# Kernel optimization log

Measured on AMD Instinct MI355X. Metric: run time of the kernel, lower is better.

## Reference

```python
import jax, jax.numpy as jnp
import numpy as np

D_MODEL = 1024
N_HEADS = 16
D_HEAD = D_MODEL // N_HEADS
EPS = 1e-5
NEG = -1.0e9


def layer_norm(x, w, b=None):
    mu = jnp.mean(x, axis=-1, keepdims=True)
    var = jnp.mean((x - mu) ** 2, axis=-1, keepdims=True)
    y = (x - mu) * jax.lax.rsqrt(var + EPS) * w
    return y + b if b is not None else y


def rope_cos_sin(L, dh, dtype):
    inv_freq = 1.0 / (10000.0 ** (jnp.arange(0, dh, 2, dtype=jnp.float32) / dh))
    freqs = jnp.arange(L, dtype=jnp.float32)[:, None] * inv_freq[None, :]  # [L, dh/2]
    emb = jnp.concatenate([freqs, freqs], axis=-1)  # [L, dh]
    return jnp.cos(emb).astype(dtype)[None, :, None, :], jnp.sin(emb).astype(dtype)[None, :, None, :]


def apply_rope(x, cos, sin):
    # x: [B, L, H, dh]; rotate_half = cat(-x2, x1)
    d = x.shape[-1] // 2
    x1, x2 = x[..., :d], x[..., d:]
    rot = jnp.concatenate([-x2, x1], axis=-1)
    return x * cos + rot * sin


def setup_inputs() -> dict:
    key = jax.random.key(0)
    ks = jax.random.split(key, 8)
    B, L, D = 2, 2048, D_MODEL
    x = jax.random.normal(ks[0], (B, L, D), dtype=jnp.float32)
    attention_mask = jnp.ones((B, L), dtype=bool)
    chain_id = jnp.sort(jax.random.randint(ks[1], (B, L), 0, 4), axis=-1).astype(jnp.int32)
    attn_bias = jax.random.normal(ks[2], (B, 1, L, L), dtype=jnp.float32) * 0.05
    s = 0.02
    return {
        "x": x,
        "attention_mask": attention_mask,
        "chain_id": chain_id,
        "attn_bias": attn_bias,
        "ln1_w": jnp.ones((D,), jnp.float32),
        "ln1_b": jnp.zeros((D,), jnp.float32),
        "Wqkv": jax.random.normal(ks[3], (D, 3 * D), jnp.float32) * s,
        "q_ln_w": jnp.ones((D,), jnp.float32),
        "k_ln_w": jnp.ones((D,), jnp.float32),
        "Wout": jax.random.normal(ks[4], (D, D), jnp.float32) * s,
    }


def reference(x, attention_mask, chain_id, attn_bias, ln1_w, ln1_b, Wqkv, q_ln_w, k_ln_w, Wout):
    B, L, D = x.shape
    H, dh = N_HEADS, D_HEAD
    # fused LN + QKV projection (Linear has no bias)
    qkv = layer_norm(x, ln1_w, ln1_b) @ Wqkv  # [B, L, 3D]
    q, k, v = jnp.split(qkv, 3, axis=-1)
    # qk layernorm (bias=False -> scale only)
    q = layer_norm(q, q_ln_w)
    k = layer_norm(k, k_ln_w)
    # rotary on [B, L, H, dh]
    q = q.reshape(B, L, H, dh)
    k = k.reshape(B, L, H, dh)
    cos, sin = rope_cos_sin(L, dh, q.dtype)
    q = apply_rope(q, cos, sin)
    k = apply_rope(k, cos, sin)
    v = v.reshape(B, L, H, dh)
    # chain mask & padding mask -> additive bias [B,1,L,L]
    mask = (chain_id[:, :, None] == chain_id[:, None, :]) \
        & attention_mask[:, :, None] & attention_mask[:, None, :]
    mask_bias = jnp.where(mask[:, None, :, :], 0.0, NEG).astype(q.dtype)
    scale = 1.0 / np.sqrt(dh)
    scores = jnp.einsum("blhd,bshd->bhls", q, k) * scale + mask_bias + attn_bias
    attn_weight = jax.nn.softmax(scores, axis=-1)  # [B,H,L,L]
    ctx = jnp.einsum("bhls,bshd->blhd", attn_weight, v).reshape(B, L, D)
    out = ctx @ Wout
    return attn_weight, out
```

## Files before the change

### kernel.cpp

```cpp
#include <hip/hip_runtime.h>


#define DEVI __device__ __forceinline__

typedef _Float16 f16;
typedef f16 f16x4 __attribute__((ext_vector_type(4)));
typedef f16 f16x8 __attribute__((ext_vector_type(8)));
typedef float f32x4 __attribute__((ext_vector_type(4)));

constexpr int Bsz = 2, Lq = 2048, Dm = 1024, Hh = 16;
constexpr int BHn = Bsz * Hh;
constexpr int ROWS = Bsz * Lq;
constexpr long long ATTN_N = (long long)BHn * Lq * Lq;

constexpr size_t OFF_XN  = 0;
constexpr size_t OFF_WQT = OFF_XN  + (size_t)4096*1024*2;
constexpr size_t OFF_WOT = OFF_WQT + (size_t)3072*1024*2;
constexpr size_t OFF_QKV = OFF_WOT + (size_t)1024*1024*2;
constexpr size_t OFF_Q   = OFF_QKV + (size_t)4096*3072*4;
constexpr size_t OFF_K   = OFF_Q   + (size_t)32*2048*64*2;
constexpr size_t OFF_VT  = OFF_K   + (size_t)32*2048*64*2;
constexpr size_t OFF_CTX = OFF_VT  + (size_t)32*64*2048*2;
constexpr size_t OFF_COS = OFF_CTX + (size_t)4096*1024*2;
constexpr size_t OFF_SIN = OFF_COS + (size_t)2048*32*4;
constexpr size_t WS_NEED = OFF_SIN + (size_t)2048*32*4;

DEVI float wsum(float v) {
#pragma unroll
  for (int o = 32; o; o >>= 1) v += __shfl_xor(v, o);
  return v;
}
DEVI float wmaxr(float v) {
#pragma unroll
  for (int o = 32; o; o >>= 1) v = fmaxf(v, __shfl_xor(v, o));
  return v;
}
DEVI f32x4 zero4() { f32x4 z; z[0]=0.f; z[1]=0.f; z[2]=0.f; z[3]=0.f; return z; }

__global__ __launch_bounds__(256) void k_ln1(const float* __restrict__ x,
    const float* __restrict__ w, const float* __restrict__ bb,
    f16* __restrict__ xn) {
  const int row = blockIdx.x, t = threadIdx.x;
  const float4 v = ((const float4*)(x + (size_t)row * Dm))[t];
  float s  = v.x + v.y + v.z + v.w;
  float s2 = v.x*v.x + v.y*v.y + v.z*v.z + v.w*v.w;
  s = wsum(s); s2 = wsum(s2);
  __shared__ float red[8];
  const int lane = t & 63, wid = t >> 6;
  if (!lane) { red[wid] = s; red[4 + wid] = s2; }
  __syncthreads();
  s  = red[0] + red[1] + red[2] + red[3];
  s2 = red[4] + red[5] + red[6] + red[7];
  const float mu = s * (1.f / Dm);
  const float rs = rsqrtf(s2 * (1.f / Dm) - mu * mu + 1e-5f);
  const float4 wv = ((const float4*)w)[t];
  const float4 bv = ((const float4*)bb)[t];
  f16x4 o;
  o[0] = (f16)((v.x - mu) * rs * wv.x + bv.x);
  o[1] = (f16)((v.y - mu) * rs * wv.y + bv.y);
  o[2] = (f16)((v.z - mu) * rs * wv.z + bv.z);
  o[3] = (f16)((v.w - mu) * rs * wv.w + bv.w);
  ((f16x4*)(xn + (size_t)row * Dm))[t] = o;
}

__global__ __launch_bounds__(256) void k_rope_tab(float* __restrict__ ct,
                                                  float* __restrict__ st) {
  const int idx = blockIdx.x * 256 + threadIdx.x;
  const int l = idx >> 5, i = idx & 31;
  const float inv = (float)(1.0 / pow(10000.0, (double)(2 * i) / 64.0));
  const float ph = (float)l * inv;
  ct[idx] = cosf(ph);
  st[idx] = sinf(ph);
}

__global__ __launch_bounds__(256) void k_transpose(const float* __restrict__ src,
    f16* __restrict__ dst, int sstride, int dstride,
    long long sbstride, long long dbstride) {
  __shared__ float tile[64][65];
  const int c0 = blockIdx.x * 64, r0 = blockIdx.y * 64;
  const float* s = src + (long long)blockIdx.z * sbstride;
  f16* d = dst + (long long)blockIdx.z * dbstride;
  const int t = threadIdx.x;
#pragma unroll
  for (int i = 0; i < 16; i++) {
    const int idx = t + i * 256, r = idx >> 6, c = idx & 63;
    tile[r][c] = s[(size_t)(r0 + r) * sstride + c0 + c];
  }
  __syncthreads();
#pragma unroll
  for (int i = 0; i < 16; i++) {
    const int idx = t + i * 256, r = idx >> 6, c = idx & 63;
    d[(size_t)(c0 + r) * dstride + r0 + c] = (f16)tile[c][r];
  }
}

template <int BM, int BN, int WR, int WC, bool AF32>
DEVI void gemm_acc(const void* __restrict__ Ag_, int lda,
                   const f16* __restrict__ Bg, int ldb, int nk,
                   char* ldsA, char* ldsB,
                   f32x4 acc[BM / WR / 16][BN / WC / 16]) {
  constexpr int MR = BM / WR / 16, NR = BN / WC / 16;
  const int t = threadIdx.x, lane = t & 63, wid = t >> 6;
  const int wr = wid / WC, wc = wid % WC;
  const int r16 = lane & 15, q = lane >> 4;
  for (int k0 = 0; k0 < nk; ++k0) {
#pragma unroll
    for (int s = 0; s < BM * 8 / 256; ++s) {
      const int sl = t + s * 256;
      const int row = sl >> 3, c16 = sl & 7;
      const int phys = (sl * 16) ^ ((row & 7) << 4);
      if constexpr (AF32) {
        const float* g = (const float*)Ag_ + (size_t)row * lda + k0 * 64 + c16 * 8;
        const float4 lo = *(const float4*)g;
        const float4 hi = *(const float4*)(g + 4);
        f16x8 h;
        h[0]=(f16)lo.x; h[1]=(f16)lo.y; h[2]=(f16)lo.z; h[3]=(f16)lo.w;
        h[4]=(f16)hi.x; h[5]=(f16)hi.y; h[6]=(f16)hi.z; h[7]=(f16)hi.w;
        *(f16x8*)(ldsA + phys) = h;
      } else {
        const f16* g = (const f16*)Ag_ + (size_t)row * lda + k0 * 64 + c16 * 8;
        *(int4*)(ldsA + phys) = *(const int4*)g;
      }
    }
#pragma unroll
    for (int s = 0; s < BN * 8 / 256; ++s) {
      const int sl = t + s * 256;
      const int row = sl >> 3, c16 = sl & 7;
      const int phys = (sl * 16) ^ ((row & 7) << 4);
      const f16* g = Bg + (size_t)row * ldb + k0 * 64 + c16 * 8;
      *(int4*)(ldsB + phys) = *(const int4*)g;
    }
    __syncthreads();
    f16x8 af[MR][2], bf[NR][2];
#pragma unroll
    for (int ks = 0; ks < 2; ++ks) {
#pragma unroll
      for (int m = 0; m < MR; m++) {
        const int row = wr * (BM / WR) + m * 16 + r16;
        const int lg = row * 128 + ks * 64 + q * 16;
        af[m][ks] = *(const f16x8*)(ldsA + (lg ^ ((row & 7) << 4)));
      }
#pragma unroll
      for (int n = 0; n < NR; n++) {
        const int row = wc * (BN / WC) + n * 16 + r16;
        const int lg = row * 128 + ks * 64 + q * 16;
        bf[n][ks] = *(const f16x8*)(ldsB + (lg ^ ((row & 7) << 4)));
      }
    }
#pragma unroll
    for (int ks = 0; ks < 2; ++ks)
#pragma unroll
      for (int m = 0; m < MR; m++)
#pragma unroll
        for (int n = 0; n < NR; n++)
          acc[m][n] = __builtin_amdgcn_mfma_f32_16x16x32_f16(af[m][ks], bf[n][ks],
                                                             acc[m][n], 0, 0, 0);
    __syncthreads();
  }
}

__global__ __launch_bounds__(256) void k_gemm_qkv(const f16* __restrict__ xn,
    const f16* __restrict__ wT, float* __restrict__ qkv) {
  __shared__ alignas(16) char lds[2 * 128 * 64 * 2];
  f32x4 acc[4][4];
#pragma unroll
  for (int m = 0; m < 4; m++)
#pragma unroll
    for (int n = 0; n < 4; n++) acc[m][n] = zero4();
  const int bm = blockIdx.x, bn = blockIdx.y;
  gemm_acc<128, 128, 2, 2, false>(xn + (size_t)bm * 128 * 1024, 1024,
                                  wT + (size_t)bn * 128 * 1024, 1024, 16,
                                  lds, lds + 128 * 64 * 2, acc);
  const int lane = threadIdx.x & 63, wid = threadIdx.x >> 6;
  const int wr = wid >> 1, wc = wid & 1;
#pragma unroll
  for (int m = 0; m < 4; m++)
#pragma unroll
    for (int n = 0; n < 4; n++) {
      const int grow = bm * 128 + wr * 64 + m * 16 + (lane >> 4) * 4;
      const int gcol = bn * 128 + wc * 64 + n * 16 + (lane & 15);
#pragma unroll
      for (int r = 0; r < 4; r++)
        qkv[(size_t)(grow + r) * 3072 + gcol] = acc[m][n][r];
    }
}

__global__ __launch_bounds__(256) void k_qkln_rope(const float* __restrict__ qkv,
    const float* __restrict__ qw, const float* __restrict__ kw,
    const float* __restrict__ ct, const float* __restrict__ st,
    f16* __restrict__ Q, f16* __restrict__ Kk) {
  const int row = blockIdx.x, t = threadIdx.x;
  const int b = row >> 11, l = row & 2047;
  const float4 qv = ((const float4*)(qkv + (size_t)row * 3072))[t];
  const float4 kv = ((const float4*)(qkv + (size_t)row * 3072 + 1024))[t];
  float qs = qv.x + qv.y + qv.z + qv.w;
  float qs2 = qv.x*qv.x + qv.y*qv.y + qv.z*qv.z + qv.w*qv.w;
  float ks_ = kv.x + kv.y + kv.z + kv.w;
  float ks2 = kv.x*kv.x + kv.y*kv.y + kv.z*kv.z + kv.w*kv.w;
  qs = wsum(qs); qs2 = wsum(qs2); ks_ = wsum(ks_); ks2 = wsum(ks2);
  __shared__ float red[16];
  const int lane = t & 63, wid = t >> 6;
  if (!lane) { red[wid] = qs; red[4+wid] = qs2; red[8+wid] = ks_; red[12+wid] = ks2; }
  __syncthreads();
  qs  = red[0]+red[1]+red[2]+red[3];   qs2 = red[4]+red[5]+red[6]+red[7];
  ks_ = red[8]+red[9]+red[10]+red[11]; ks2 = red[12]+red[13]+red[14]+red[15];
  const float qmu = qs * (1.f/1024), qrs = rsqrtf(qs2*(1.f/1024) - qmu*qmu + 1e-5f);
  const float kmu = ks_ * (1.f/1024), krs = rsqrtf(ks2*(1.f/1024) - kmu*kmu + 1e-5f);
  __shared__ float qn[1024], kn[1024];
  const float4 qwv = ((const float4*)qw)[t], kwv = ((const float4*)kw)[t];
  float4 qnn, knn;
  qnn.x = (qv.x-qmu)*qrs*qwv.x; qnn.y = (qv.y-qmu)*qrs*qwv.y;
  qnn.z = (qv.z-qmu)*qrs*qwv.z; qnn.w = (qv.w-qmu)*qrs*qwv.w;
  knn.x = (kv.x-kmu)*krs*kwv.x; knn.y = (kv.y-kmu)*krs*kwv.y;
  knn.z = (kv.z-kmu)*krs*kwv.z; knn.w = (kv.w-kmu)*krs*kwv.w;
  ((float4*)qn)[t] = qnn;
  ((float4*)kn)[t] = knn;
  __syncthreads();
  const int d0 = 4 * t, h = d0 >> 6, dd0 = d0 & 63;
  f16x4 qo, ko;
#pragma unroll
  for (int j = 0; j < 4; j++) {
    const int d = d0 + j, dd = d & 63, p = dd & 31;
    const float c = ct[l * 32 + p], s = st[l * 32 + p];
    const float q1 = qn[d], k1 = kn[d];
    const float qr = (dd < 32) ? -qn[d + 32] : qn[d - 32];
    const float kr = (dd < 32) ? -kn[d + 32] : kn[d - 32];
    qo[j] = (f16)(q1 * c + qr * s);
    ko[j] = (f16)(k1 * c + kr * s);
  }
  const size_t base = (((size_t)(b * 16 + h) * 2048) + l) * 64 + dd0;
  *(f16x4*)(Q + base) = qo;
  *(f16x4*)(Kk + base) = ko;
}

__global__ __launch_bounds__(256) void k_gemm_scores(const f16* __restrict__ Q,
    const f16* __restrict__ Kk, const int* __restrict__ chain,
    const float* __restrict__ bias, float* __restrict__ attn) {
  __shared__ alignas(16) char lds[2 * 128 * 64 * 2];
  __shared__ int cidr[128], cidc[128];
  f32x4 acc[4][4];
#pragma unroll
  for (int m = 0; m < 4; m++)
#pragma unroll
    for (int n = 0; n < 4; n++) acc[m][n] = zero4();
  const int bm = blockIdx.x, bn = blockIdx.y, bh = blockIdx.z;
  const int b = bh >> 4;
  gemm_acc<128, 128, 2, 2, false>(Q + ((size_t)bh * 2048 + bm * 128) * 64, 64,
                                  Kk + ((size_t)bh * 2048 + bn * 128) * 64, 64, 1,
                                  lds, lds + 128 * 64 * 2, acc);
  const int t = threadIdx.x;
  if (t < 128) cidr[t] = chain[b * 2048 + bm * 128 + t];
  else cidc[t - 128] = chain[b * 2048 + bn * 128 + (t - 128)];
  __syncthreads();
  const int lane = t & 63, wid = t >> 6, wr = wid >> 1, wc = wid & 1;
#pragma unroll
  for (int m = 0; m < 4; m++)
#pragma unroll
    for (int n = 0; n < 4; n++) {
      const int lr0 = wr * 64 + m * 16 + (lane >> 4) * 4;
      const int lc = wc * 64 + n * 16 + (lane & 15);
      const int s = bn * 128 + lc;
      const int cs = cidc[lc];
#pragma unroll
      for (int r = 0; r < 4; r++) {
        const int l = bm * 128 + lr0 + r;
        float v = acc[m][n][r] * 0.125f + bias[((size_t)b * 2048 + l) * 2048 + s];
        if (cidr[lr0 + r] != cs) v -= 1e9f;
        attn[((size_t)bh * 2048 + l) * 2048 + s] = v;
      }
    }
}

__global__ __launch_bounds__(256) void k_softmax(float* __restrict__ attn) {
  float* p = attn + (size_t)blockIdx.x * 2048;
  const int t = threadIdx.x;
  float4 a0 = ((const float4*)p)[t];
  float4 a1 = ((const float4*)p)[t + 256];
  float m = fmaxf(fmaxf(fmaxf(a0.x, a0.y), fmaxf(a0.z, a0.w)),
                  fmaxf(fmaxf(a1.x, a1.y), fmaxf(a1.z, a1.w)));
  m = wmaxr(m);
  __shared__ float red[4];
  const int lane = t & 63, wid = t >> 6;
  if (!lane) red[wid] = m;
  __syncthreads();
  m = fmaxf(fmaxf(red[0], red[1]), fmaxf(red[2], red[3]));
  float4 e0, e1;
  e0.x = __expf(a0.x - m); e0.y = __expf(a0.y - m);
  e0.z = __expf(a0.z - m); e0.w = __expf(a0.w - m);
  e1.x = __expf(a1.x - m); e1.y = __expf(a1.y - m);
  e1.z = __expf(a1.z - m); e1.w = __expf(a1.w - m);
  float s = e0.x+e0.y+e0.z+e0.w + e1.x+e1.y+e1.z+e1.w;
  s = wsum(s);
  __syncthreads();
  if (!lane) red[wid] = s;
  __syncthreads();
  s = red[0] + red[1] + red[2] + red[3];
  const float inv = 1.f / s;
  e0.x *= inv; e0.y *= inv; e0.z *= inv; e0.w *= inv;
  e1.x *= inv; e1.y *= inv; e1.z *= inv; e1.w *= inv;
  ((float4*)p)[t] = e0;
  ((float4*)p)[t + 256] = e1;
}

__global__ __launch_bounds__(256) void k_gemm_pv(const float* __restrict__ attn,
    const f16* __restrict__ Vt, f16* __restrict__ ctx) {
  __shared__ alignas(16) char lds[128 * 64 * 2 + 64 * 64 * 2];
  f32x4 acc[2][4];
#pragma unroll
  for (int m = 0; m < 2; m++)
#pragma unroll
    for (int n = 0; n < 4; n++) acc[m][n] = zero4();
  const int bm = blockIdx.x, bh = blockIdx.z;
  gemm_acc<128, 64, 4, 1, true>(attn + ((size_t)bh * 2048 + bm * 128) * 2048, 2048,
                                Vt + (size_t)bh * 64 * 2048, 2048, 32,
                                lds, lds + 128 * 64 * 2, acc);
  const int lane = threadIdx.x & 63, wid = threadIdx.x >> 6;
  const int b = bh >> 4, h = bh & 15;
#pragma unroll
  for (int m = 0; m < 2; m++)
#pragma unroll
    for (int n = 0; n < 4; n++) {
      const int l0 = bm * 128 + wid * 32 + m * 16 + (lane >> 4) * 4;
      const int dd = n * 16 + (lane & 15);
#pragma unroll
      for (int r = 0; r < 4; r++)
        ctx[(((size_t)b * 2048 + (l0 + r)) * 16 + h) * 64 + dd] = (f16)acc[m][n][r];
    }
}

__global__ __launch_bounds__(256) void k_gemm_proj(const f16* __restrict__ ctx,
    const f16* __restrict__ wT, float* __restrict__ out) {
  __shared__ alignas(16) char lds[2 * 128 * 64 * 2];
  f32x4 acc[4][4];
#pragma unroll
  for (int m = 0; m < 4; m++)
#pragma unroll
    for (int n = 0; n < 4; n++) acc[m][n] = zero4();
  const int bm = blockIdx.x, bn = blockIdx.y;
  gemm_acc<128, 128, 2, 2, false>(ctx + (size_t)bm * 128 * 1024, 1024,
                                  wT + (size_t)bn * 128 * 1024, 1024, 16,
                                  lds, lds + 128 * 64 * 2, acc);
  const int lane = threadIdx.x & 63, wid = threadIdx.x >> 6;
  const int wr = wid >> 1, wc = wid & 1;
#pragma unroll
  for (int m = 0; m < 4; m++)
#pragma unroll
    for (int n = 0; n < 4; n++) {
      const int grow = bm * 128 + wr * 64 + m * 16 + (lane >> 4) * 4;
      const int gcol = bn * 128 + wc * 64 + n * 16 + (lane & 15);
#pragma unroll
      for (int r = 0; r < 4; r++)
        out[(size_t)(grow + r) * 1024 + gcol] = acc[m][n][r];
    }
}

extern "C" void kernel_launch(void* const* d_in, const int* in_sizes, int n_in,
                              void* d_out, int out_size, void* d_ws, size_t ws_size,
                              hipStream_t stream) {
  const float* x    = (const float*)d_in[0];
  const int*   chain = (const int*)d_in[2];
  const float* bias = (const float*)d_in[3];
  const float* ln1w = (const float*)d_in[4];
  const float* ln1b = (const float*)d_in[5];
  const float* wqkv = (const float*)d_in[6];
  const float* qlnw = (const float*)d_in[7];
  const float* klnw = (const float*)d_in[8];
  const float* wout = (const float*)d_in[9];

  float* attn = (float*)d_out;
  float* outp = attn + ATTN_N;

  char* ws = (char*)d_ws;
  f16*   xn    = (f16*)(ws + OFF_XN);
  f16*   wqkvT = (f16*)(ws + OFF_WQT);
  f16*   woutT = (f16*)(ws + OFF_WOT);
  float* qkv   = (float*)(ws + OFF_QKV);
  f16*   Qh    = (f16*)(ws + OFF_Q);
  f16*   Kh    = (f16*)(ws + OFF_K);
  f16*   Vt    = (f16*)(ws + OFF_VT);
  f16*   ctx   = (f16*)(ws + OFF_CTX);
  float* ct    = (float*)(ws + OFF_COS);
  float* st    = (float*)(ws + OFF_SIN);

  k_ln1<<<ROWS, 256, 0, stream>>>(x, ln1w, ln1b, xn);
  k_rope_tab<<<(2048 * 32) / 256, 256, 0, stream>>>(ct, st);
  k_transpose<<<dim3(3072 / 64, 1024 / 64, 1), 256, 0, stream>>>(
      wqkv, wqkvT, 3072, 1024, 0, 0);
  k_transpose<<<dim3(1024 / 64, 1024 / 64, 1), 256, 0, stream>>>(
      wout, woutT, 1024, 1024, 0, 0);
  k_gemm_qkv<<<dim3(4096 / 128, 3072 / 128), 256, 0, stream>>>(xn, wqkvT, qkv);
  k_qkln_rope<<<ROWS, 256, 0, stream>>>(qkv, qlnw, klnw, ct, st, Qh, Kh);
  k_transpose<<<dim3(1024 / 64, 2048 / 64, 2), 256, 0, stream>>>(
      qkv + 2048, Vt, 3072, 2048, (long long)2048 * 3072, (long long)1024 * 2048);
  k_gemm_scores<<<dim3(16, 16, 32), 256, 0, stream>>>(Qh, Kh, chain, bias, attn);
  k_softmax<<<BHn * Lq, 256, 0, stream>>>(attn);
  k_gemm_pv<<<dim3(16, 1, 32), 256, 0, stream>>>(attn, Vt, ctx);
  k_gemm_proj<<<dim3(4096 / 128, 1024 / 128), 256, 0, stream>>>(ctx, woutT, outp);
}
```

Measured before the change: 1.111 ms.

## Fuse score computation and softmax into two-pass online max/sum attention kernels

Replaces the scores GEMM plus separate softmax kernel with two kernels. The first streams K tiles to compute the per-row running max and sum online. The second recomputes QK, applies bias and mask, and writes normalized probabilities directly. This removes the write-then-read-then-write round trip of the full fp32 score matrix, in exchange for computing QK and reading bias twice. It also uses a much smaller grid with a serial loop over key tiles.

```diff
diff --git a/kernel.cpp b/kernel.cpp
--- a/kernel.cpp
+++ b/kernel.cpp
@@ -23,16 +23,12 @@
 constexpr size_t OFF_CTX = OFF_VT  + (size_t)32*64*2048*2;
 constexpr size_t OFF_COS = OFF_CTX + (size_t)4096*1024*2;
 constexpr size_t OFF_SIN = OFF_COS + (size_t)2048*32*4;
-constexpr size_t WS_NEED = OFF_SIN + (size_t)2048*32*4;
+constexpr size_t OFF_M   = OFF_SIN + (size_t)2048*32*4;
+constexpr size_t OFF_L   = OFF_M   + (size_t)32*2048*4;
 
 DEVI float wsum(float v) {
 #pragma unroll
   for (int o = 32; o; o >>= 1) v += __shfl_xor(v, o);
-  return v;
-}
-DEVI float wmaxr(float v) {
-#pragma unroll
-  for (int o = 32; o; o >>= 1) v = fmaxf(v, __shfl_xor(v, o));
   return v;
 }
 DEVI f32x4 zero4() { f32x4 z; z[0]=0.f; z[1]=0.f; z[2]=0.f; z[3]=0.f; return z; }
@@ -233,73 +229,151 @@
   *(f16x4*)(Kk + base) = ko;
 }
 
-__global__ __launch_bounds__(256) void k_gemm_scores(const f16* __restrict__ Q,
-    const f16* __restrict__ Kk, const int* __restrict__ chain,
-    const float* __restrict__ bias, float* __restrict__ attn) {
-  __shared__ alignas(16) char lds[2 * 128 * 64 * 2];
+DEVI void stage_tile64(const f16* __restrict__ g, char* lds) {
+  const int t = threadIdx.x;
+#pragma unroll
+  for (int s = 0; s < 4; ++s) {
+    const int sl = t + s * 256;
+    const int row = sl >> 3, c16 = sl & 7;
+    const int phys = (sl * 16) ^ ((row & 7) << 4);
+    *(int4*)(lds + phys) = *(const int4*)(g + (size_t)row * 64 + c16 * 8);
+  }
+}
+DEVI f16x8 ldsfrag(const char* lds, int row, int ks, int q) {
+  const int lg = row * 128 + ks * 64 + q * 16;
+  return *(const f16x8*)(lds + (lg ^ ((row & 7) << 4)));
+}
+DEVI void attn_qk_tile(const char* ldsQ, const char* ldsK, int wid, int lo, int q,
+                       f32x4 acc[2][8]) {
+#pragma unroll
+  for (int m = 0; m < 2; m++)
+#pragma unroll
+    for (int n = 0; n < 8; n++) acc[m][n] = zero4();
+#pragma unroll
+  for (int ks = 0; ks < 2; ++ks) {
+    const f16x8 a0 = ldsfrag(ldsQ, wid * 32 + lo, ks, q);
+    const f16x8 a1 = ldsfrag(ldsQ, wid * 32 + 16 + lo, ks, q);
+#pragma unroll
+    for (int n = 0; n < 8; ++n) {
+      const f16x8 bf = ldsfrag(ldsK, n * 16 + lo, ks, q);
+      acc[0][n] = __builtin_amdgcn_mfma_f32_16x16x32_f16(a0, bf, acc[0][n], 0, 0, 0);
+      acc[1][n] = __builtin_amdgcn_mfma_f32_16x16x32_f16(a1, bf, acc[1][n], 0, 0, 0);
+    }
+  }
+}
+
+__global__ __launch_bounds__(256) void k_attn_ml(const f16* __restrict__ Qh,
+    const f16* __restrict__ Kh, const int* __restrict__ chain,
+    const float* __restrict__ bias, float* __restrict__ marr,
+    float* __restrict__ larr) {
+  __shared__ alignas(16) char ldsQ[128 * 64 * 2];
+  __shared__ alignas(16) char ldsK[128 * 64 * 2];
   __shared__ int cidr[128], cidc[128];
-  f32x4 acc[4][4];
-#pragma unroll
-  for (int m = 0; m < 4; m++)
-#pragma unroll
-    for (int n = 0; n < 4; n++) acc[m][n] = zero4();
-  const int bm = blockIdx.x, bn = blockIdx.y, bh = blockIdx.z;
-  const int b = bh >> 4;
-  gemm_acc<128, 128, 2, 2, false>(Q + ((size_t)bh * 2048 + bm * 128) * 64, 64,
-                                  Kk + ((size_t)bh * 2048 + bn * 128) * 64, 64, 1,
-                                  lds, lds + 128 * 64 * 2, acc);
-  const int t = threadIdx.x;
+  const int bm = blockIdx.x, bh = blockIdx.y, b = bh >> 4;
+  const int t = threadIdx.x, lane = t & 63, wid = t >> 6;
+  const int lo = lane & 15, q = lane >> 4;
+  stage_tile64(Qh + ((size_t)bh * 2048 + bm * 128) * 64, ldsQ);
   if (t < 128) cidr[t] = chain[b * 2048 + bm * 128 + t];
-  else cidc[t - 128] = chain[b * 2048 + bn * 128 + (t - 128)];
-  __syncthreads();
-  const int lane = t & 63, wid = t >> 6, wr = wid >> 1, wc = wid & 1;
-#pragma unroll
-  for (int m = 0; m < 4; m++)
-#pragma unroll
-    for (int n = 0; n < 4; n++) {
-      const int lr0 = wr * 64 + m * 16 + (lane >> 4) * 4;
-      const int lc = wc * 64 + n * 16 + (lane & 15);
-      const int s = bn * 128 + lc;
-      const int cs = cidc[lc];
+  float mr[2][4], lr[2][4];
+#pragma unroll
+  for (int m = 0; m < 2; m++)
+#pragma unroll
+    for (int r = 0; r < 4; r++) { mr[m][r] = -__builtin_inff(); lr[m][r] = 0.f; }
+  for (int bn = 0; bn < 16; ++bn) {
+    __syncthreads();
+    stage_tile64(Kh + ((size_t)bh * 2048 + bn * 128) * 64, ldsK);
+    if (t < 128) cidc[t] = chain[b * 2048 + bn * 128 + t];
+    __syncthreads();
+    f32x4 acc[2][8];
+    attn_qk_tile(ldsQ, ldsK, wid, lo, q, acc);
+    const int s0 = bn * 128;
+#pragma unroll
+    for (int m = 0; m < 2; m++)
 #pragma unroll
       for (int r = 0; r < 4; r++) {
-        const int l = bm * 128 + lr0 + r;
-        float v = acc[m][n][r] * 0.125f + bias[((size_t)b * 2048 + l) * 2048 + s];
-        if (cidr[lr0 + r] != cs) v -= 1e9f;
-        attn[((size_t)bh * 2048 + l) * 2048 + s] = v;
-      }
-    }
-}
-
-__global__ __launch_bounds__(256) void k_softmax(float* __restrict__ attn) {
-  float* p = attn + (size_t)blockIdx.x * 2048;
-  const int t = threadIdx.x;
-  float4 a0 = ((const float4*)p)[t];
-  float4 a1 = ((const float4*)p)[t + 256];
-  float m = fmaxf(fmaxf(fmaxf(a0.x, a0.y), fmaxf(a0.z, a0.w)),
-                  fmaxf(fmaxf(a1.x, a1.y), fmaxf(a1.z, a1.w)));
-  m = wmaxr(m);
-  __shared__ float red[4];
-  const int lane = t & 63, wid = t >> 6;
-  if (!lane) red[wid] = m;
-  __syncthreads();
-  m = fmaxf(fmaxf(red[0], red[1]), fmaxf(red[2], red[3]));
-  float4 e0, e1;
-  e0.x = __expf(a0.x - m); e0.y = __expf(a0.y - m);
-  e0.z = __expf(a0.z - m); e0.w = __expf(a0.w - m);
-  e1.x = __expf(a1.x - m); e1.y = __expf(a1.y - m);
-  e1.z = __expf(a1.z - m); e1.w = __expf(a1.w - m);
-  float s = e0.x+e0.y+e0.z+e0.w + e1.x+e1.y+e1.z+e1.w;
-  s = wsum(s);
-  __syncthreads();
-  if (!lane) red[wid] = s;
-  __syncthreads();
-  s = red[0] + red[1] + red[2] + red[3];
-  const float inv = 1.f / s;
-  e0.x *= inv; e0.y *= inv; e0.z *= inv; e0.w *= inv;
-  e1.x *= inv; e1.y *= inv; e1.z *= inv; e1.w *= inv;
-  ((float4*)p)[t] = e0;
-  ((float4*)p)[t + 256] = e1;
+        const int lloc = wid * 32 + m * 16 + q * 4 + r;
+        const int l = bm * 128 + lloc;
+        const int cr = cidr[lloc];
+        const float* bp = bias + ((size_t)b * 2048 + l) * 2048 + s0 + lo;
+        float lg[8];
+        float tmax = -__builtin_inff();
+#pragma unroll
+        for (int n = 0; n < 8; ++n) {
+          float v = acc[m][n][r] * 0.125f + bp[n * 16];
+          if (cr != cidc[n * 16 + lo]) v -= 1e9f;
+          lg[n] = v;
+          tmax = fmaxf(tmax, v);
+        }
+#pragma unroll
+        for (int o = 1; o < 16; o <<= 1) tmax = fmaxf(tmax, __shfl_xor(tmax, o));
+        const float nm = fmaxf(mr[m][r], tmax);
+        float ss = 0.f;
+#pragma unroll
+        for (int n = 0; n < 8; ++n) ss += __expf(lg[n] - nm);
+#pragma unroll
+        for (int o = 1; o < 16; o <<= 1) ss += __shfl_xor(ss, o);
+        lr[m][r] = lr[m][r] * __expf(mr[m][r] - nm) + ss;
+        mr[m][r] = nm;
+      }
+  }
+  if (lo == 0) {
+#pragma unroll
+    for (int m = 0; m < 2; m++)
+#pragma unroll
+      for (int r = 0; r < 4; r++) {
+        const int l = bm * 128 + wid * 32 + m * 16 + q * 4 + r;
+        marr[(size_t)bh * 2048 + l] = mr[m][r];
+        larr[(size_t)bh * 2048 + l] = lr[m][r];
+      }
+  }
+}
+
+__global__ __launch_bounds__(256) void k_attn_pw(const f16* __restrict__ Qh,
+    const f16* __restrict__ Kh, const int* __restrict__ chain,
+    const float* __restrict__ bias, const float* __restrict__ marr,
+    const float* __restrict__ larr, float* __restrict__ attn) {
+  __shared__ alignas(16) char ldsQ[128 * 64 * 2];
+  __shared__ alignas(16) char ldsK[128 * 64 * 2];
+  __shared__ int cidr[128], cidc[128];
+  const int bm = blockIdx.x, bh = blockIdx.y, b = bh >> 4;
+  const int t = threadIdx.x, lane = t & 63, wid = t >> 6;
+  const int lo = lane & 15, q = lane >> 4;
+  stage_tile64(Qh + ((size_t)bh * 2048 + bm * 128) * 64, ldsQ);
+  if (t < 128) cidr[t] = chain[b * 2048 + bm * 128 + t];
+  float mr[2][4], il[2][4];
+#pragma unroll
+  for (int m = 0; m < 2; m++)
+#pragma unroll
+    for (int r = 0; r < 4; r++) {
+      const int l = bm * 128 + wid * 32 + m * 16 + q * 4 + r;
+      mr[m][r] = marr[(size_t)bh * 2048 + l];
+      il[m][r] = 1.f / larr[(size_t)bh * 2048 + l];
+    }
+  for (int bn = 0; bn < 16; ++bn) {
+    __syncthreads();
+    stage_tile64(Kh + ((size_t)bh * 2048 + bn * 128) * 64, ldsK);
+    if (t < 128) cidc[t] = chain[b * 2048 + bn * 128 + t];
+    __syncthreads();
+    f32x4 acc[2][8];
+    attn_qk_tile(ldsQ, ldsK, wid, lo, q, acc);
+    const int s0 = bn * 128;
+#pragma unroll
+    for (int m = 0; m < 2; m++)
+#pragma unroll
+      for (int r = 0; r < 4; r++) {
+        const int lloc = wid * 32 + m * 16 + q * 4 + r;
+        const int l = bm * 128 + lloc;
+        const int cr = cidr[lloc];
+        const float* bp = bias + ((size_t)b * 2048 + l) * 2048 + s0 + lo;
+        float* op = attn + ((size_t)bh * 2048 + l) * 2048 + s0 + lo;
+#pragma unroll
+        for (int n = 0; n < 8; ++n) {
+          float v = acc[m][n][r] * 0.125f + bp[n * 16];
+          if (cr != cidc[n * 16 + lo]) v -= 1e9f;
+          op[n * 16] = __expf(v - mr[m][r]) * il[m][r];
+        }
+      }
+  }
 }
 
 __global__ __launch_bounds__(256) void k_gemm_pv(const float* __restrict__ attn,
@@ -381,6 +455,8 @@
   f16*   ctx   = (f16*)(ws + OFF_CTX);
   float* ct    = (float*)(ws + OFF_COS);
   float* st    = (float*)(ws + OFF_SIN);
+  float* marr  = (float*)(ws + OFF_M);
+  float* larr  = (float*)(ws + OFF_L);
 
   k_ln1<<<ROWS, 256, 0, stream>>>(x, ln1w, ln1b, xn);
   k_rope_tab<<<(2048 * 32) / 256, 256, 0, stream>>>(ct, st);
@@ -392,8 +468,8 @@
   k_qkln_rope<<<ROWS, 256, 0, stream>>>(qkv, qlnw, klnw, ct, st, Qh, Kh);
   k_transpose<<<dim3(1024 / 64, 2048 / 64, 2), 256, 0, stream>>>(
       qkv + 2048, Vt, 3072, 2048, (long long)2048 * 3072, (long long)1024 * 2048);
-  k_gemm_scores<<<dim3(16, 16, 32), 256, 0, stream>>>(Qh, Kh, chain, bias, attn);
-  k_softmax<<<BHn * Lq, 256, 0, stream>>>(attn);
+  k_attn_ml<<<dim3(16, 32), 256, 0, stream>>>(Qh, Kh, chain, bias, marr, larr);
+  k_attn_pw<<<dim3(16, 32), 256, 0, stream>>>(Qh, Kh, chain, bias, marr, larr, attn);
   k_gemm_pv<<<dim3(16, 1, 32), 256, 0, stream>>>(attn, Vt, ctx);
   k_gemm_proj<<<dim3(4096 / 128, 1024 / 128), 256, 0, stream>>>(ctx, woutT, outp);
 }
```

After: 1.340 ms. 20.6% more time.

## Fuse scores, softmax and PV into two-pass flash-style attention kernels

Applied to the files above, without the earlier changes.

Replaces the separate scores GEMM, softmax and PV GEMM with two kernels. The first computes the per-row running max and sum, and the second recomputes scores, writes the normalized attention weights once, and accumulates P·V in registers. This removes the round trips that write, reread and rewrite the large fp32 attention matrix. The cost is recomputing QK^T, and both new kernels read K, V and the bias straight from global memory without LDS staging, with a grid of only 512 blocks. It also swaps the MFMA operand order so GEMM epilogues can store float4 rows, and routes ctx through fp32 into the projection.

```diff
diff --git a/kernel.cpp b/kernel.cpp
--- a/kernel.cpp
+++ b/kernel.cpp
@@ -17,25 +17,33 @@
 constexpr size_t OFF_WQT = OFF_XN  + (size_t)4096*1024*2;
 constexpr size_t OFF_WOT = OFF_WQT + (size_t)3072*1024*2;
 constexpr size_t OFF_QKV = OFF_WOT + (size_t)1024*1024*2;
+constexpr size_t OFF_CTXF = OFF_QKV;
 constexpr size_t OFF_Q   = OFF_QKV + (size_t)4096*3072*4;
 constexpr size_t OFF_K   = OFF_Q   + (size_t)32*2048*64*2;
 constexpr size_t OFF_VT  = OFF_K   + (size_t)32*2048*64*2;
-constexpr size_t OFF_CTX = OFF_VT  + (size_t)32*64*2048*2;
-constexpr size_t OFF_COS = OFF_CTX + (size_t)4096*1024*2;
+constexpr size_t OFF_COS = OFF_VT  + (size_t)32*64*2048*2;
 constexpr size_t OFF_SIN = OFF_COS + (size_t)2048*32*4;
-constexpr size_t WS_NEED = OFF_SIN + (size_t)2048*32*4;
+constexpr size_t OFF_M   = OFF_SIN + (size_t)2048*32*4;
+constexpr size_t OFF_L   = OFF_M   + (size_t)32*2048*4;
 
 DEVI float wsum(float v) {
 #pragma unroll
   for (int o = 32; o; o >>= 1) v += __shfl_xor(v, o);
   return v;
 }
-DEVI float wmaxr(float v) {
-#pragma unroll
-  for (int o = 32; o; o >>= 1) v = fmaxf(v, __shfl_xor(v, o));
-  return v;
-}
 DEVI f32x4 zero4() { f32x4 z; z[0]=0.f; z[1]=0.f; z[2]=0.f; z[3]=0.f; return z; }
+
+DEVI f32x4 mfma32(f16x8 a, f16x8 b, f32x4 c) {
+  return __builtin_amdgcn_mfma_f32_16x16x32_f16(a, b, c, 0, 0, 0);
+}
+DEVI f32x4 mfma16(f16x4 a, f16x4 b, f32x4 c) {
+#if __has_builtin(__builtin_amdgcn_mfma_f32_16x16x16f16)
+  return __builtin_amdgcn_mfma_f32_16x16x16f16(a, b, c, 0, 0, 0);
+#else
+  asm volatile("v_mfma_f32_16x16x16_f16 %0, %1, %2, %0" : "+v"(c) : "v"(a), "v"(b));
+  return c;
+#endif
+}
 
 __global__ __launch_bounds__(256) void k_ln1(const float* __restrict__ x,
     const float* __restrict__ w, const float* __restrict__ bb,
@@ -153,8 +161,7 @@
       for (int m = 0; m < MR; m++)
 #pragma unroll
         for (int n = 0; n < NR; n++)
-          acc[m][n] = __builtin_amdgcn_mfma_f32_16x16x32_f16(af[m][ks], bf[n][ks],
-                                                             acc[m][n], 0, 0, 0);
+          acc[m][n] = mfma32(bf[n][ks], af[m][ks], acc[m][n]);
     __syncthreads();
   }
 }
@@ -173,15 +180,17 @@
                                   lds, lds + 128 * 64 * 2, acc);
   const int lane = threadIdx.x & 63, wid = threadIdx.x >> 6;
   const int wr = wid >> 1, wc = wid & 1;
+  const int xr = lane & 15, q4 = lane >> 4;
 #pragma unroll
   for (int m = 0; m < 4; m++)
 #pragma unroll
     for (int n = 0; n < 4; n++) {
-      const int grow = bm * 128 + wr * 64 + m * 16 + (lane >> 4) * 4;
-      const int gcol = bn * 128 + wc * 64 + n * 16 + (lane & 15);
-#pragma unroll
-      for (int r = 0; r < 4; r++)
-        qkv[(size_t)(grow + r) * 3072 + gcol] = acc[m][n][r];
+      const int grow = bm * 128 + wr * 64 + m * 16 + xr;
+      const int gcol = bn * 128 + wc * 64 + n * 16 + q4 * 4;
+      float4 st4;
+      st4.x = acc[m][n][0]; st4.y = acc[m][n][1];
+      st4.z = acc[m][n][2]; st4.w = acc[m][n][3];
+      *(float4*)(qkv + (size_t)grow * 3072 + gcol) = st4;
     }
 }
 
@@ -233,102 +242,161 @@
   *(f16x4*)(Kk + base) = ko;
 }
 
-__global__ __launch_bounds__(256) void k_gemm_scores(const f16* __restrict__ Q,
-    const f16* __restrict__ Kk, const int* __restrict__ chain,
-    const float* __restrict__ bias, float* __restrict__ attn) {
-  __shared__ alignas(16) char lds[2 * 128 * 64 * 2];
-  __shared__ int cidr[128], cidc[128];
-  f32x4 acc[4][4];
-#pragma unroll
-  for (int m = 0; m < 4; m++)
-#pragma unroll
-    for (int n = 0; n < 4; n++) acc[m][n] = zero4();
-  const int bm = blockIdx.x, bn = blockIdx.y, bh = blockIdx.z;
-  const int b = bh >> 4;
-  gemm_acc<128, 128, 2, 2, false>(Q + ((size_t)bh * 2048 + bm * 128) * 64, 64,
-                                  Kk + ((size_t)bh * 2048 + bn * 128) * 64, 64, 1,
-                                  lds, lds + 128 * 64 * 2, acc);
-  const int t = threadIdx.x;
-  if (t < 128) cidr[t] = chain[b * 2048 + bm * 128 + t];
-  else cidc[t - 128] = chain[b * 2048 + bn * 128 + (t - 128)];
-  __syncthreads();
-  const int lane = t & 63, wid = t >> 6, wr = wid >> 1, wc = wid & 1;
-#pragma unroll
-  for (int m = 0; m < 4; m++)
-#pragma unroll
-    for (int n = 0; n < 4; n++) {
-      const int lr0 = wr * 64 + m * 16 + (lane >> 4) * 4;
-      const int lc = wc * 64 + n * 16 + (lane & 15);
-      const int s = bn * 128 + lc;
-      const int cs = cidc[lc];
-#pragma unroll
-      for (int r = 0; r < 4; r++) {
-        const int l = bm * 128 + lr0 + r;
-        float v = acc[m][n][r] * 0.125f + bias[((size_t)b * 2048 + l) * 2048 + s];
-        if (cidr[lr0 + r] != cs) v -= 1e9f;
-        attn[((size_t)bh * 2048 + l) * 2048 + s] = v;
-      }
-    }
-}
-
-__global__ __launch_bounds__(256) void k_softmax(float* __restrict__ attn) {
-  float* p = attn + (size_t)blockIdx.x * 2048;
-  const int t = threadIdx.x;
-  float4 a0 = ((const float4*)p)[t];
-  float4 a1 = ((const float4*)p)[t + 256];
-  float m = fmaxf(fmaxf(fmaxf(a0.x, a0.y), fmaxf(a0.z, a0.w)),
-                  fmaxf(fmaxf(a1.x, a1.y), fmaxf(a1.z, a1.w)));
-  m = wmaxr(m);
-  __shared__ float red[4];
-  const int lane = t & 63, wid = t >> 6;
-  if (!lane) red[wid] = m;
-  __syncthreads();
-  m = fmaxf(fmaxf(red[0], red[1]), fmaxf(red[2], red[3]));
-  float4 e0, e1;
-  e0.x = __expf(a0.x - m); e0.y = __expf(a0.y - m);
-  e0.z = __expf(a0.z - m); e0.w = __expf(a0.w - m);
-  e1.x = __expf(a1.x - m); e1.y = __expf(a1.y - m);
-  e1.z = __expf(a1.z - m); e1.w = __expf(a1.w - m);
-  float s = e0.x+e0.y+e0.z+e0.w + e1.x+e1.y+e1.z+e1.w;
-  s = wsum(s);
-  __syncthreads();
-  if (!lane) red[wid] = s;
-  __syncthreads();
-  s = red[0] + red[1] + red[2] + red[3];
-  const float inv = 1.f / s;
-  e0.x *= inv; e0.y *= inv; e0.z *= inv; e0.w *= inv;
-  e1.x *= inv; e1.y *= inv; e1.z *= inv; e1.w *= inv;
-  ((float4*)p)[t] = e0;
-  ((float4*)p)[t + 256] = e1;
-}
-
-__global__ __launch_bounds__(256) void k_gemm_pv(const float* __restrict__ attn,
-    const f16* __restrict__ Vt, f16* __restrict__ ctx) {
-  __shared__ alignas(16) char lds[128 * 64 * 2 + 64 * 64 * 2];
-  f32x4 acc[2][4];
+__global__ __launch_bounds__(256) void k_attn_ml(const f16* __restrict__ Qh,
+    const f16* __restrict__ Kh, const int* __restrict__ chain,
+    const float* __restrict__ bias, float* __restrict__ marr,
+    float* __restrict__ larr) {
+  const int bm = blockIdx.x, bh = blockIdx.y, b = bh >> 4;
+  const int t = threadIdx.x, lane = t & 63, wid = t >> 6;
+  const int lo = lane & 15, q4 = lane >> 4;
+  const f16* Qb = Qh + (size_t)bh * 2048 * 64;
+  const f16* Kb = Kh + (size_t)bh * 2048 * 64;
+  const int* chb = chain + b * 2048;
+  f16x8 qf[2][2];
+  int cidr[2];
+  const float* brow[2];
+#pragma unroll
+  for (int m = 0; m < 2; m++) {
+    const int qrow = bm * 128 + wid * 32 + m * 16 + lo;
+#pragma unroll
+    for (int ks = 0; ks < 2; ks++)
+      qf[m][ks] = *(const f16x8*)(Qb + (size_t)qrow * 64 + ks * 32 + q4 * 8);
+    cidr[m] = chb[qrow];
+    brow[m] = bias + ((size_t)b * 2048 + qrow) * 2048;
+  }
+  float lm[2] = {-3.0e38f, -3.0e38f}, lr[2] = {0.f, 0.f};
+  for (int bn = 0; bn < 16; ++bn) {
+#pragma unroll 2
+    for (int n = 0; n < 8; ++n) {
+      const int kbase = bn * 128 + n * 16;
+      const f16x8 kf0 = *(const f16x8*)(Kb + (size_t)(kbase + lo) * 64 + q4 * 8);
+      const f16x8 kf1 = *(const f16x8*)(Kb + (size_t)(kbase + lo) * 64 + 32 + q4 * 8);
+      const int4 cc = *(const int4*)(chb + kbase + q4 * 4);
+      f32x4 s0 = zero4(), s1 = zero4();
+      s0 = mfma32(kf0, qf[0][0], s0); s0 = mfma32(kf1, qf[0][1], s0);
+      s1 = mfma32(kf0, qf[1][0], s1); s1 = mfma32(kf1, qf[1][1], s1);
+#pragma unroll
+      for (int m = 0; m < 2; m++) {
+        const f32x4 sa = m ? s1 : s0;
+        const float4 b4 = *(const float4*)(brow[m] + kbase + q4 * 4);
+        float v0 = sa[0] * 0.125f + b4.x; if (cc.x != cidr[m]) v0 -= 1e9f;
+        float v1 = sa[1] * 0.125f + b4.y; if (cc.y != cidr[m]) v1 -= 1e9f;
+        float v2 = sa[2] * 0.125f + b4.z; if (cc.z != cidr[m]) v2 -= 1e9f;
+        float v3 = sa[3] * 0.125f + b4.w; if (cc.w != cidr[m]) v3 -= 1e9f;
+        const float tm = fmaxf(fmaxf(v0, v1), fmaxf(v2, v3));
+        const float nm = fmaxf(lm[m], tm);
+        const float ss = __expf(v0 - nm) + __expf(v1 - nm) +
+                         __expf(v2 - nm) + __expf(v3 - nm);
+        lr[m] = lr[m] * __expf(lm[m] - nm) + ss;
+        lm[m] = nm;
+      }
+    }
+  }
+#pragma unroll
+  for (int off = 16; off <= 32; off <<= 1) {
+#pragma unroll
+    for (int m = 0; m < 2; m++) {
+      const float om = __shfl_xor(lm[m], off);
+      const float ol = __shfl_xor(lr[m], off);
+      const float nm = fmaxf(lm[m], om);
+      lr[m] = lr[m] * __expf(lm[m] - nm) + ol * __expf(om - nm);
+      lm[m] = nm;
+    }
+  }
+  if (q4 == 0) {
+#pragma unroll
+    for (int m = 0; m < 2; m++) {
+      const int qrow = bm * 128 + wid * 32 + m * 16 + lo;
+      marr[(size_t)bh * 2048 + qrow] = lm[m];
+      larr[(size_t)bh * 2048 + qrow] = lr[m];
+    }
+  }
+}
+
+__global__ __launch_bounds__(256) void k_attn_fused(const f16* __restrict__ Qh,
+    const f16* __restrict__ Kh, const f16* __restrict__ Vt,
+    const int* __restrict__ chain, const float* __restrict__ bias,
+    const float* __restrict__ marr, const float* __restrict__ larr,
+    float* __restrict__ attn, float* __restrict__ ctxf) {
+  const int bm = blockIdx.x, bh = blockIdx.y, b = bh >> 4, h = bh & 15;
+  const int t = threadIdx.x, lane = t & 63, wid = t >> 6;
+  const int lo = lane & 15, q4 = lane >> 4;
+  const f16* Qb = Qh + (size_t)bh * 2048 * 64;
+  const f16* Kb = Kh + (size_t)bh * 2048 * 64;
+  const f16* Vb = Vt + (size_t)bh * 64 * 2048;
+  const int* chb = chain + b * 2048;
+  f16x8 qf[2][2];
+  int cidr[2];
+  const float* brow[2];
+  float* prow[2];
+  float mr[2], il[2];
+#pragma unroll
+  for (int m = 0; m < 2; m++) {
+    const int qrow = bm * 128 + wid * 32 + m * 16 + lo;
+#pragma unroll
+    for (int ks = 0; ks < 2; ks++)
+      qf[m][ks] = *(const f16x8*)(Qb + (size_t)qrow * 64 + ks * 32 + q4 * 8);
+    cidr[m] = chb[qrow];
+    brow[m] = bias + ((size_t)b * 2048 + qrow) * 2048;
+    prow[m] = attn + ((size_t)bh * 2048 + qrow) * 2048;
+    mr[m] = marr[(size_t)bh * 2048 + qrow];
+    il[m] = 1.f / larr[(size_t)bh * 2048 + qrow];
+  }
+  f32x4 cacc[2][4];
 #pragma unroll
   for (int m = 0; m < 2; m++)
 #pragma unroll
-    for (int n = 0; n < 4; n++) acc[m][n] = zero4();
-  const int bm = blockIdx.x, bh = blockIdx.z;
-  gemm_acc<128, 64, 4, 1, true>(attn + ((size_t)bh * 2048 + bm * 128) * 2048, 2048,
-                                Vt + (size_t)bh * 64 * 2048, 2048, 32,
-                                lds, lds + 128 * 64 * 2, acc);
-  const int lane = threadIdx.x & 63, wid = threadIdx.x >> 6;
-  const int b = bh >> 4, h = bh & 15;
+    for (int dt = 0; dt < 4; dt++) cacc[m][dt] = zero4();
+  for (int bn = 0; bn < 16; ++bn) {
+#pragma unroll 2
+    for (int n = 0; n < 8; ++n) {
+      const int kbase = bn * 128 + n * 16;
+      const f16x8 kf0 = *(const f16x8*)(Kb + (size_t)(kbase + lo) * 64 + q4 * 8);
+      const f16x8 kf1 = *(const f16x8*)(Kb + (size_t)(kbase + lo) * 64 + 32 + q4 * 8);
+      const int4 cc = *(const int4*)(chb + kbase + q4 * 4);
+      f32x4 s0 = zero4(), s1 = zero4();
+      s0 = mfma32(kf0, qf[0][0], s0); s0 = mfma32(kf1, qf[0][1], s0);
+      s1 = mfma32(kf0, qf[1][0], s1); s1 = mfma32(kf1, qf[1][1], s1);
+      f16x4 pa[2];
+#pragma unroll
+      for (int m = 0; m < 2; m++) {
+        const f32x4 sa = m ? s1 : s0;
+        const float4 b4 = *(const float4*)(brow[m] + kbase + q4 * 4);
+        float v0 = sa[0] * 0.125f + b4.x; if (cc.x != cidr[m]) v0 -= 1e9f;
+        float v1 = sa[1] * 0.125f + b4.y; if (cc.y != cidr[m]) v1 -= 1e9f;
+        float v2 = sa[2] * 0.125f + b4.z; if (cc.z != cidr[m]) v2 -= 1e9f;
+        float v3 = sa[3] * 0.125f + b4.w; if (cc.w != cidr[m]) v3 -= 1e9f;
+        float4 p4;
+        p4.x = __expf(v0 - mr[m]) * il[m];
+        p4.y = __expf(v1 - mr[m]) * il[m];
+        p4.z = __expf(v2 - mr[m]) * il[m];
+        p4.w = __expf(v3 - mr[m]) * il[m];
+        *(float4*)(prow[m] + kbase + q4 * 4) = p4;
+        f16x4 pc;
+        pc[0] = (f16)p4.x; pc[1] = (f16)p4.y; pc[2] = (f16)p4.z; pc[3] = (f16)p4.w;
+        pa[m] = pc;
+      }
+#pragma unroll
+      for (int dt = 0; dt < 4; dt++) {
+        const f16x4 vf = *(const f16x4*)(Vb + (size_t)(dt * 16 + lo) * 2048 + kbase + q4 * 4);
+        cacc[0][dt] = mfma16(pa[0], vf, cacc[0][dt]);
+        cacc[1][dt] = mfma16(pa[1], vf, cacc[1][dt]);
+      }
+    }
+  }
 #pragma unroll
   for (int m = 0; m < 2; m++)
 #pragma unroll
-    for (int n = 0; n < 4; n++) {
-      const int l0 = bm * 128 + wid * 32 + m * 16 + (lane >> 4) * 4;
-      const int dd = n * 16 + (lane & 15);
+    for (int dt = 0; dt < 4; dt++) {
+      const int l0 = bm * 128 + wid * 32 + m * 16 + q4 * 4;
 #pragma unroll
       for (int r = 0; r < 4; r++)
-        ctx[(((size_t)b * 2048 + (l0 + r)) * 16 + h) * 64 + dd] = (f16)acc[m][n][r];
-    }
-}
-
-__global__ __launch_bounds__(256) void k_gemm_proj(const f16* __restrict__ ctx,
+        ctxf[((size_t)b * 2048 + l0 + r) * 1024 + h * 64 + dt * 16 + lo] =
+            cacc[m][dt][r];
+    }
+}
+
+__global__ __launch_bounds__(256) void k_gemm_proj(const float* __restrict__ ctxf,
     const f16* __restrict__ wT, float* __restrict__ out) {
   __shared__ alignas(16) char lds[2 * 128 * 64 * 2];
   f32x4 acc[4][4];
@@ -337,20 +405,22 @@
 #pragma unroll
     for (int n = 0; n < 4; n++) acc[m][n] = zero4();
   const int bm = blockIdx.x, bn = blockIdx.y;
-  gemm_acc<128, 128, 2, 2, false>(ctx + (size_t)bm * 128 * 1024, 1024,
-                                  wT + (size_t)bn * 128 * 1024, 1024, 16,
-                                  lds, lds + 128 * 64 * 2, acc);
+  gemm_acc<128, 128, 2, 2, true>(ctxf + (size_t)bm * 128 * 1024, 1024,
+                                 wT + (size_t)bn * 128 * 1024, 1024, 16,
+                                 lds, lds + 128 * 64 * 2, acc);
   const int lane = threadIdx.x & 63, wid = threadIdx.x >> 6;
   const int wr = wid >> 1, wc = wid & 1;
+  const int xr = lane & 15, q4 = lane >> 4;
 #pragma unroll
   for (int m = 0; m < 4; m++)
 #pragma unroll
     for (int n = 0; n < 4; n++) {
-      const int grow = bm * 128 + wr * 64 + m * 16 + (lane >> 4) * 4;
-      const int gcol = bn * 128 + wc * 64 + n * 16 + (lane & 15);
-#pragma unroll
-      for (int r = 0; r < 4; r++)
-        out[(size_t)(grow + r) * 1024 + gcol] = acc[m][n][r];
+      const int grow = bm * 128 + wr * 64 + m * 16 + xr;
+      const int gcol = bn * 128 + wc * 64 + n * 16 + q4 * 4;
+      float4 st4;
+      st4.x = acc[m][n][0]; st4.y = acc[m][n][1];
+      st4.z = acc[m][n][2]; st4.w = acc[m][n][3];
+      *(float4*)(out + (size_t)grow * 1024 + gcol) = st4;
     }
 }
 
@@ -375,12 +445,14 @@
   f16*   wqkvT = (f16*)(ws + OFF_WQT);
   f16*   woutT = (f16*)(ws + OFF_WOT);
   float* qkv   = (float*)(ws + OFF_QKV);
+  float* ctxf  = (float*)(ws + OFF_CTXF);
   f16*   Qh    = (f16*)(ws + OFF_Q);
   f16*   Kh    = (f16*)(ws + OFF_K);
   f16*   Vt    = (f16*)(ws + OFF_VT);
-  f16*   ctx   = (f16*)(ws + OFF_CTX);
   float* ct    = (float*)(ws + OFF_COS);
   float* st    = (float*)(ws + OFF_SIN);
+  float* marr  = (float*)(ws + OFF_M);
+  float* larr  = (float*)(ws + OFF_L);
 
   k_ln1<<<ROWS, 256, 0, stream>>>(x, ln1w, ln1b, xn);
   k_rope_tab<<<(2048 * 32) / 256, 256, 0, stream>>>(ct, st);
@@ -392,8 +464,8 @@
   k_qkln_rope<<<ROWS, 256, 0, stream>>>(qkv, qlnw, klnw, ct, st, Qh, Kh);
   k_transpose<<<dim3(1024 / 64, 2048 / 64, 2), 256, 0, stream>>>(
       qkv + 2048, Vt, 3072, 2048, (long long)2048 * 3072, (long long)1024 * 2048);
-  k_gemm_scores<<<dim3(16, 16, 32), 256, 0, stream>>>(Qh, Kh, chain, bias, attn);
-  k_softmax<<<BHn * Lq, 256, 0, stream>>>(attn);
-  k_gemm_pv<<<dim3(16, 1, 32), 256, 0, stream>>>(attn, Vt, ctx);
-  k_gemm_proj<<<dim3(4096 / 128, 1024 / 128), 256, 0, stream>>>(ctx, woutT, outp);
-}
+  k_attn_ml<<<dim3(16, 32), 256, 0, stream>>>(Qh, Kh, chain, bias, marr, larr);
+  k_attn_fused<<<dim3(16, 32), 256, 0, stream>>>(Qh, Kh, Vt, chain, bias,
+                                                 marr, larr, attn, ctxf);
+  k_gemm_proj<<<dim3(4096 / 128, 1024 / 128), 256, 0, stream>>>(ctxf, woutT, outp);
+}
```

Result: faster. 1.080 ms (-2.8%).
